# Kernel tuning notes

Hardware: AMD Instinct MI355X
Metric: run time of the kernel (lower is better)

Reference implementation:

```python
import jax, jax.numpy as jnp
import numpy as np

VOC_SIZE = 100000
EMB_SIZE = 300
BATCH = 262144


def setup_inputs() -> dict:
    key = jax.random.key(0)
    k1, k2, k3, k4, k5, k6, k7, k8 = jax.random.split(key, 8)
    center = jax.random.randint(k1, (BATCH, 1), 0, VOC_SIZE)
    outside = jax.random.randint(k2, (BATCH, 1), 0, VOC_SIZE)
    coocs = jax.random.uniform(k3, (BATCH, 1), dtype=jnp.float32)
    weighting = jax.random.uniform(k4, (BATCH, 1), dtype=jnp.float32)
    center_embedding = jax.random.normal(k5, (VOC_SIZE, EMB_SIZE), dtype=jnp.float32)
    outside_embedding = jax.random.normal(k6, (VOC_SIZE, EMB_SIZE), dtype=jnp.float32)
    center_bias = jax.random.normal(k7, (VOC_SIZE, 1), dtype=jnp.float32)
    outside_bias = jax.random.normal(k8, (VOC_SIZE, 1), dtype=jnp.float32)
    return {
        "center": center,
        "outside": outside,
        "coocs": coocs,
        "weighting": weighting,
        "center_embedding": center_embedding,
        "outside_embedding": outside_embedding,
        "center_bias": center_bias,
        "outside_bias": outside_bias,
    }


def reference(center, outside, coocs, weighting,
              center_embedding, outside_embedding,
              center_bias, outside_bias):
    c_idx = center[:, 0]    # [B]
    o_idx = outside[:, 0]   # [B]
    center_embeds = center_embedding[c_idx]     # [B, E]
    outside_embeds = outside_embedding[o_idx]   # [B, E]
    c_bias = center_bias[c_idx]                 # [B, 1]
    o_bias = outside_bias[o_idx]                # [B, 1]
    # per-sample dot product, keepdims to match [B, 1]
    inner = jnp.sum(center_embeds * outside_embeds, axis=-1, keepdims=True)  # [B, 1]
    err = inner + c_bias + o_bias - coocs
    loss = jnp.sum(weighting * err * err)
    return loss
```

## Files before the change

kernel.cpp:

```cpp
#include <hip/hip_runtime.h>

#define BATCH 262144
#define EMB 300
#define NBLK 4096

__global__ __launch_bounds__(256) void glove_main(
    const int*   __restrict__ center,
    const int*   __restrict__ outside,
    const float* __restrict__ coocs,
    const float* __restrict__ weighting,
    const float* __restrict__ cemb,
    const float* __restrict__ oemb,
    const float* __restrict__ cbias,
    const float* __restrict__ obias,
    float*       __restrict__ block_sums)
{
    const int tid  = threadIdx.x;
    const int warp = tid >> 6;
    const int lane = tid & 63;
    const int l4   = lane & 3;
    const int pg   = lane >> 2;
    const int p    = (blockIdx.x * 4 + warp) * 16 + pg;

    const int   ci = center[p];
    const int   oi = outside[p];
    const float cc = coocs[p];
    const float wt = weighting[p];
    const float cb = cbias[ci];
    const float ob = obias[oi];

    const float4* __restrict__ A = (const float4*)(cemb + (long)ci * EMB);
    const float4* __restrict__ B = (const float4*)(oemb + (long)oi * EMB);

    float acc = 0.0f;
    #pragma unroll
    for (int k = 0; k < 18; ++k) {
        float4 a = A[l4 + 4 * k];
        float4 b = B[l4 + 4 * k];
        acc += a.x * b.x + a.y * b.y + a.z * b.z + a.w * b.w;
    }
    if (l4 < 3) {
        float4 a = A[72 + l4];
        float4 b = B[72 + l4];
        acc += a.x * b.x + a.y * b.y + a.z * b.z + a.w * b.w;
    }

    acc += __shfl_xor(acc, 1);
    acc += __shfl_xor(acc, 2);

    const float e = acc + cb + ob - cc;
    float local = (l4 == 0) ? wt * e * e : 0.0f;

    #pragma unroll
    for (int off = 32; off > 0; off >>= 1)
        local += __shfl_down(local, off, 64);

    __shared__ float smem[4];
    if (lane == 0) smem[warp] = local;
    __syncthreads();
    if (tid == 0)
        block_sums[blockIdx.x] = smem[0] + smem[1] + smem[2] + smem[3];
}

__global__ __launch_bounds__(1024) void glove_reduce(
    const float* __restrict__ part, float* __restrict__ out)
{
    const int t = threadIdx.x;
    float4 v = ((const float4*)part)[t];
    float s = v.x + v.y + v.z + v.w;
    #pragma unroll
    for (int off = 32; off > 0; off >>= 1)
        s += __shfl_down(s, off, 64);
    __shared__ float sm[16];
    if ((t & 63) == 0) sm[t >> 6] = s;
    __syncthreads();
    if (t < 16) {
        float x = sm[t];
        #pragma unroll
        for (int off = 8; off > 0; off >>= 1)
            x += __shfl_down(x, off, 16);
        if (t == 0) out[0] = x;
    }
}

extern "C" void kernel_launch(void* const* d_in, const int* in_sizes, int n_in,
                              void* d_out, int out_size, void* d_ws, size_t ws_size,
                              hipStream_t stream) {
    const int*   center    = (const int*)  d_in[0];
    const int*   outside   = (const int*)  d_in[1];
    const float* coocs     = (const float*)d_in[2];
    const float* weighting = (const float*)d_in[3];
    const float* cemb      = (const float*)d_in[4];
    const float* oemb      = (const float*)d_in[5];
    const float* cbias     = (const float*)d_in[6];
    const float* obias     = (const float*)d_in[7];
    float* out        = (float*)d_out;
    float* block_sums = (float*)d_ws;

    glove_main<<<NBLK, 256, 0, stream>>>(
        center, outside, coocs, weighting, cemb, oemb, cbias, obias, block_sums);
    glove_reduce<<<1, 1024, 0, stream>>>(block_sums, out);
}
```

Before: 311.1 us.

## Split embedding dot product into two column-half passes for cache locality

Splits the gather-and-dot kernel into two passes, each covering half the embedding columns, with the first pass writing per-sample partial dot products to workspace. The aim is to shrink the working set of randomly gathered embedding rows per pass so more of it stays resident in the large last-level cache. It adds a kernel launch, re-reads of indices, and a partial-sum buffer round trip.

```diff
diff --git a/kernel.cpp b/kernel.cpp
--- a/kernel.cpp
+++ b/kernel.cpp
@@ -3,8 +3,46 @@
 #define BATCH 262144
 #define EMB 300
 #define NBLK 4096
+#define OFF2 152
 
-__global__ __launch_bounds__(256) void glove_main(
+__global__ __launch_bounds__(256) void glove_pass1(
+    const int*   __restrict__ center,
+    const int*   __restrict__ outside,
+    const float* __restrict__ cemb,
+    const float* __restrict__ oemb,
+    float*       __restrict__ partial)
+{
+    const int tid  = threadIdx.x;
+    const int warp = tid >> 6;
+    const int lane = tid & 63;
+    const int l4   = lane & 3;
+    const int pg   = lane >> 2;
+    const int p    = (blockIdx.x * 4 + warp) * 16 + pg;
+
+    const int ci = center[p];
+    const int oi = outside[p];
+    const float4* __restrict__ A = (const float4*)(cemb + (long)ci * EMB);
+    const float4* __restrict__ B = (const float4*)(oemb + (long)oi * EMB);
+
+    float acc = 0.0f;
+    #pragma unroll
+    for (int k = 0; k < 9; ++k) {
+        float4 a = A[l4 + 4 * k];
+        float4 b = B[l4 + 4 * k];
+        acc += a.x * b.x + a.y * b.y + a.z * b.z + a.w * b.w;
+    }
+    if (l4 < 2) {
+        float4 a = A[36 + l4];
+        float4 b = B[36 + l4];
+        acc += a.x * b.x + a.y * b.y + a.z * b.z + a.w * b.w;
+    }
+
+    acc += __shfl_xor(acc, 1);
+    acc += __shfl_xor(acc, 2);
+    if (l4 == 0) partial[p] = acc;
+}
+
+__global__ __launch_bounds__(256) void glove_pass2(
     const int*   __restrict__ center,
     const int*   __restrict__ outside,
     const float* __restrict__ coocs,
@@ -13,6 +51,7 @@
     const float* __restrict__ oemb,
     const float* __restrict__ cbias,
     const float* __restrict__ obias,
+    const float* __restrict__ partial,
     float*       __restrict__ block_sums)
 {
     const int tid  = threadIdx.x;
@@ -22,35 +61,38 @@
     const int pg   = lane >> 2;
     const int p    = (blockIdx.x * 4 + warp) * 16 + pg;
 
-    const int   ci = center[p];
-    const int   oi = outside[p];
+    const int ci = center[p];
+    const int oi = outside[p];
+    const float4* __restrict__ A = (const float4*)(cemb + (long)ci * EMB + OFF2);
+    const float4* __restrict__ B = (const float4*)(oemb + (long)oi * EMB + OFF2);
+
     const float cc = coocs[p];
     const float wt = weighting[p];
     const float cb = cbias[ci];
     const float ob = obias[oi];
-
-    const float4* __restrict__ A = (const float4*)(cemb + (long)ci * EMB);
-    const float4* __restrict__ B = (const float4*)(oemb + (long)oi * EMB);
+    const float pp = partial[p];
 
     float acc = 0.0f;
     #pragma unroll
-    for (int k = 0; k < 18; ++k) {
+    for (int k = 0; k < 9; ++k) {
         float4 a = A[l4 + 4 * k];
         float4 b = B[l4 + 4 * k];
         acc += a.x * b.x + a.y * b.y + a.z * b.z + a.w * b.w;
     }
-    if (l4 < 3) {
-        float4 a = A[72 + l4];
-        float4 b = B[72 + l4];
+    if (l4 == 0) {
+        float4 a = A[36];
+        float4 b = B[36];
         acc += a.x * b.x + a.y * b.y + a.z * b.z + a.w * b.w;
     }
 
     acc += __shfl_xor(acc, 1);
     acc += __shfl_xor(acc, 2);
 
-    const float e = acc + cb + ob - cc;
-    float local = (l4 == 0) ? wt * e * e : 0.0f;
-
+    float local = 0.0f;
+    if (l4 == 0) {
+        const float e = acc + pp + cb + ob - cc;
+        local = wt * e * e;
+    }
     #pragma unroll
     for (int off = 32; off > 0; off >>= 1)
         local += __shfl_down(local, off, 64);
@@ -94,10 +136,15 @@
     const float* oemb      = (const float*)d_in[5];
     const float* cbias     = (const float*)d_in[6];
     const float* obias     = (const float*)d_in[7];
-    float* out        = (float*)d_out;
-    float* block_sums = (float*)d_ws;
+    float* out = (float*)d_out;
 
-    glove_main<<<NBLK, 256, 0, stream>>>(
-        center, outside, coocs, weighting, cemb, oemb, cbias, obias, block_sums);
+    char* ws = (char*)d_ws;
+    float* partial    = (float*)ws;
+    float* block_sums = (float*)(ws + (size_t)BATCH * 4);
+
+    glove_pass1<<<NBLK, 256, 0, stream>>>(center, outside, cemb, oemb, partial);
+    glove_pass2<<<NBLK, 256, 0, stream>>>(center, outside, coocs, weighting,
+                                          cemb, oemb, cbias, obias, partial,
+                                          block_sums);
     glove_reduce<<<1, 1024, 0, stream>>>(block_sums, out);
 }
```

Result: no change. 313.4 us (+0.7%).
